# Optimization experiments

Measured on AMD Instinct MI355X. Metric: run time of the kernel, lower is better.

The kernel has to match this reference:

```python
import jax, jax.numpy as jnp
import numpy as np
import math

D_MODEL = 768
HEADS = 12
D_FF = 3072
B, S = 2, 2048


def layer_norm(x, g, b, eps=1e-6):
    mu = jnp.mean(x, axis=-1, keepdims=True)
    var = jnp.mean((x - mu) ** 2, axis=-1, keepdims=True)
    return (x - mu) / jnp.sqrt(var + eps) * g + b


def gelu_tanh(x):
    c = math.sqrt(2.0 / math.pi)
    return 0.5 * x * (1.0 + jnp.tanh(c * (x + 0.044715 * x ** 3)))


def setup_inputs() -> dict:
    key = jax.random.key(0)
    ks = jax.random.split(key, 12)
    s = 0.02
    inp = {
        "iter": 1,
        "query": jax.random.normal(ks[0], (B, S, D_MODEL), jnp.float32),
        "inputs": jax.random.normal(ks[1], (B, S, D_MODEL), jnp.float32),
        "mask": jax.random.randint(ks[2], (B, S), 0, 2).astype(bool),
        "Wq": jax.random.normal(ks[3], (D_MODEL, D_MODEL), jnp.float32) * s,
        "bq": jnp.zeros((D_MODEL,), jnp.float32),
        "Wk": jax.random.normal(ks[4], (D_MODEL, D_MODEL), jnp.float32) * s,
        "bk": jnp.zeros((D_MODEL,), jnp.float32),
        "Wv": jax.random.normal(ks[5], (D_MODEL, D_MODEL), jnp.float32) * s,
        "bv": jnp.zeros((D_MODEL,), jnp.float32),
        "Wo": jax.random.normal(ks[6], (D_MODEL, D_MODEL), jnp.float32) * s,
        "bo": jnp.zeros((D_MODEL,), jnp.float32),
        "ln1_g": jnp.ones((D_MODEL,), jnp.float32),
        "ln1_b": jnp.zeros((D_MODEL,), jnp.float32),
        "W1": jax.random.normal(ks[7], (D_MODEL, D_FF), jnp.float32) * s,
        "b1": jnp.zeros((D_FF,), jnp.float32),
        "W2": jax.random.normal(ks[8], (D_FF, D_MODEL), jnp.float32) * s,
        "b2": jnp.zeros((D_MODEL,), jnp.float32),
        "ln2_g": jnp.ones((D_MODEL,), jnp.float32),
        "ln2_b": jnp.zeros((D_MODEL,), jnp.float32),
    }
    return inp


def reference(iter, query, inputs, mask, Wq, bq, Wk, bk, Wv, bv, Wo, bo,
              ln1_g, ln1_b, W1, b1, W2, b2, ln2_g, ln2_b):
    dh = D_MODEL // HEADS
    # pre-LN (skipped when iter == 0)
    x = layer_norm(inputs, ln1_g, ln1_b) if iter != 0 else inputs
    # QKV projections -> [B, H, S, dh]
    def heads(t):
        return t.reshape(B, S, HEADS, dh).transpose(0, 2, 1, 3)
    q = heads(x @ Wq + bq) / math.sqrt(dh)
    k = heads(x @ Wk + bk)
    v = heads(x @ Wv + bv)
    scores = jnp.einsum("bhqd,bhkd->bhqk", q, k)
    scores = jnp.where(mask[:, None, None, :], -1e18, scores)
    attn = jax.nn.softmax(scores, axis=-1)
    ctx = jnp.einsum("bhqk,bhkd->bhqd", attn, v)
    ctx = ctx.transpose(0, 2, 1, 3).reshape(B, S, D_MODEL)
    attn_out = ctx @ Wo + bo
    out = attn_out + inputs  # dropout=0 -> identity
    # FFN with residual pre-LN and tanh-GELU
    h = layer_norm(out, ln2_g, ln2_b)
    inter = gelu_tanh(h @ W1 + b1)
    return inter @ W2 + b2 + out
```

## Files before the change

### kernel.cpp

```cpp
#include <hip/hip_runtime.h>
#include <hip/hip_bf16.h>
#include <stdint.h>

#define D_MODEL 768
#define HEADS   12
#define DHEAD   64
#define D_FF    3072
#define BB      2
#define SS      2048
#define MTOT    (BB*SS)

typedef uint16_t u16;
typedef uint32_t u32;
typedef __attribute__((ext_vector_type(8))) short short8;
typedef __attribute__((ext_vector_type(4))) short short4v;
typedef __attribute__((ext_vector_type(4))) float f32x4;
typedef __attribute__((ext_vector_type(16))) float f32x16;
typedef __attribute__((ext_vector_type(2))) unsigned uint2v;

__device__ __forceinline__ u16 f2bf(float f) {
    union { float f; u32 u; } v; v.f = f;
    u32 r = v.u + 0x7fffu + ((v.u >> 16) & 1u);
    return (u16)(r >> 16);
}

__device__ __forceinline__ float bf2f(u16 u) {
    union { u32 u; float f; } v; v.u = ((u32)u) << 16;
    return v.f;
}

__device__ __forceinline__ u32 cvtpk(float a, float b) {
    u32 r;
    asm("v_cvt_pk_bf16_f32 %0, %1, %2" : "=v"(r) : "v"(a), "v"(b));
    return r;
}

__device__ __forceinline__ void plswap(u32& a, u32& b, int hi) {
#if __has_builtin(__builtin_amdgcn_permlane32_swap)
    uint2v r = __builtin_amdgcn_permlane32_swap(a, b, false, false);
    a = r[0]; b = r[1];
#else
    u32 ax = (u32)__shfl_xor((int)a, 32), bx = (u32)__shfl_xor((int)b, 32);
    u32 na = hi ? bx : a, nb = hi ? b : ax;
    a = na; b = nb;
#endif
}

__device__ __forceinline__ void gload16(const void* g, void* l) {
    __builtin_amdgcn_global_load_lds(
        (const __attribute__((address_space(1))) u32*)g,
        (__attribute__((address_space(3))) u32*)l, 16, 0, 0);
}

#define MFMA16(a, b, c) __builtin_amdgcn_mfma_f32_16x16x32_bf16((a), (b), (c), 0, 0, 0)
#define MFMA32(a, b, c) __builtin_amdgcn_mfma_f32_32x32x16_bf16((a), (b), (c), 0, 0, 0)

__device__ __forceinline__ float gelu_tanh_f(float x) {
    float x3 = x * x * x;
    return 0.5f * x * (1.0f + tanhf(0.7978845608028654f * (x + 0.044715f * x3)));
}

__global__ __launch_bounds__(256)
void transpose_cast(const float* __restrict__ W, u16* __restrict__ Wt, int R, int C) {
    __shared__ float tile[32][33];
    int bx = blockIdx.x, by = blockIdx.y;
    int x = threadIdx.x & 31, y0 = threadIdx.x >> 5;
#pragma unroll
    for (int i = 0; i < 4; ++i) {
        int y = y0 + i * 8;
        tile[y][x] = W[(size_t)(by * 32 + y) * C + bx * 32 + x];
    }
    __syncthreads();
#pragma unroll
    for (int i = 0; i < 4; ++i) {
        int y = y0 + i * 8;
        Wt[(size_t)(bx * 32 + y) * R + by * 32 + x] = f2bf(tile[x][y]);
    }
}

__global__ void maskprep(const int* __restrict__ m, float* __restrict__ mf, int n) {
    int i = blockIdx.x * 256 + threadIdx.x;
    if (i < n) mf[i] = m[i] ? -1e30f : 0.0f;
}

__global__ __launch_bounds__(256)
void ln_bf16(const float* __restrict__ in, const float* __restrict__ g,
             const float* __restrict__ bta, u16* __restrict__ out,
             const int* __restrict__ iterp, int checkIter) {
    int row = blockIdx.x, tid = threadIdx.x;
    const float* x = in + (size_t)row * D_MODEL;
    float v0 = x[tid], v1 = x[tid + 256], v2 = x[tid + 512];
    float s = v0 + v1 + v2;
    float s2 = v0 * v0 + v1 * v1 + v2 * v2;
#pragma unroll
    for (int o = 1; o < 64; o <<= 1) { s += __shfl_xor(s, o); s2 += __shfl_xor(s2, o); }
    __shared__ float sh[8];
    int w = tid >> 6;
    if ((tid & 63) == 0) { sh[w] = s; sh[4 + w] = s2; }
    __syncthreads();
    s = sh[0] + sh[1] + sh[2] + sh[3];
    s2 = sh[4] + sh[5] + sh[6] + sh[7];
    float mu = s * (1.0f / 768.0f);
    float var = s2 * (1.0f / 768.0f) - mu * mu;
    float rstd = rsqrtf(var + 1e-6f);
    bool skip = checkIter && (iterp[0] == 0);
    u16* o0 = out + (size_t)row * D_MODEL;
    if (skip) {
        o0[tid] = f2bf(v0); o0[tid + 256] = f2bf(v1); o0[tid + 512] = f2bf(v2);
    } else {
        o0[tid]       = f2bf((v0 - mu) * rstd * g[tid]       + bta[tid]);
        o0[tid + 256] = f2bf((v1 - mu) * rstd * g[tid + 256] + bta[tid + 256]);
        o0[tid + 512] = f2bf((v2 - mu) * rstd * g[tid + 512] + bta[tid + 512]);
    }
}

template <int MODE>
__global__ __launch_bounds__(256, 3)
void gemm_bt(const u16* __restrict__ A, const u16* __restrict__ Bt,
             int K, int N,
             const float* __restrict__ bias0, const float* __restrict__ bias1,
             const float* __restrict__ bias2,
             const float* __restrict__ res,
             float* __restrict__ outF, u16* __restrict__ oq,
             u16* __restrict__ ok, u16* __restrict__ ov) {
    __shared__ __align__(16) u16 aT[3][128 * 32];
    __shared__ __align__(16) u16 bT[3][128 * 32];
    const int tid = threadIdx.x;
    const int lane = tid & 63;
    const int w = tid >> 6;
    const int wr = w >> 1, wc = w & 1;
    const int lm = lane & 15, lq = lane >> 4;
    const int bm = blockIdx.y, bn = blockIdx.x;
    const int kzlen = K / gridDim.z;
    const int kbeg = blockIdx.z * kzlen;
    const int nsteps = kzlen >> 5;

    const u16* Abase = A  + (size_t)(bm * 128) * K + kbeg;
    const u16* Bbase = Bt + (size_t)(bn * 128) * K + kbeg;

    auto stage = [&](int buf, int t) {
        int k0 = t * 32;
#pragma unroll
        for (int j = 0; j < 2; ++j) {
            int d = j * 256 + tid;
            int row = d >> 2, p = d & 3;
            int src = (p ^ (row & 3)) * 8;
            gload16(Abase + (size_t)row * K + k0 + src, aT[buf] + (j * 256 + w * 64) * 8);
            gload16(Bbase + (size_t)row * K + k0 + src, bT[buf] + (j * 256 + w * 64) * 8);
        }
    };

    f32x4 acc[4][4] = {};
    stage(0, 0);
    if (nsteps > 1) stage(1, 1);

#pragma unroll 1
    for (int t = 0; t < nsteps; ++t) {
        if (t + 1 < nsteps) asm volatile("s_waitcnt vmcnt(4)" ::: "memory");
        else                asm volatile("s_waitcnt vmcnt(0)" ::: "memory");
        __syncthreads();
        const u16* Ab = aT[t % 3];
        const u16* Bb = bT[t % 3];
        short8 av[4], bv[4];
#pragma unroll
        for (int m = 0; m < 4; ++m) {
            int row = wr * 64 + m * 16 + lm;
            av[m] = *(const short8*)(Ab + row * 32 + ((lq ^ (row & 3)) * 8));
        }
#pragma unroll
        for (int n = 0; n < 4; ++n) {
            int row = wc * 64 + n * 16 + lm;
            bv[n] = *(const short8*)(Bb + row * 32 + ((lq ^ (row & 3)) * 8));
        }
#pragma unroll
        for (int m = 0; m < 4; ++m)
#pragma unroll
            for (int n = 0; n < 4; ++n)
                acc[m][n] = MFMA16(av[m], bv[n], acc[m][n]);
        if (t + 2 < nsteps) stage((t + 2) % 3, t + 2);
    }

#pragma unroll
    for (int m = 0; m < 4; ++m) {
#pragma unroll
        for (int n = 0; n < 4; ++n) {
            int col = bn * 128 + wc * 64 + n * 16 + lm;
#pragma unroll
            for (int r = 0; r < 4; ++r) {
                int row = bm * 128 + wr * 64 + m * 16 + lq * 4 + r;
                float v = acc[m][n][r];
                if (MODE == 0) {
                    int proj = col / D_MODEL;
                    int d = col - proj * D_MODEL;
                    int hh = d >> 6, dhi = d & 63;
                    int bb = row >> 11, sIdx = row & 2047;
                    if (proj == 0) {
                        v = (v + bias0[d]) * 0.18033688011112042f;
                        oq[((size_t)(bb * HEADS + hh) * SS + sIdx) * DHEAD + dhi] = f2bf(v);
                    } else if (proj == 1) {
                        v = v + bias1[d];
                        ok[((size_t)(bb * HEADS + hh) * SS + sIdx) * DHEAD + dhi] = f2bf(v);
                    } else {
                        v = v + bias2[d];
                        ov[((size_t)(bb * HEADS + hh) * DHEAD + dhi) * SS + sIdx] = f2bf(v);
                    }
                } else if (MODE == 1) {
                    if (gridDim.z > 1) {
                        outF[((size_t)blockIdx.z * MTOT + row) * N + col] = v;
                    } else {
                        size_t idx = (size_t)row * N + col;
                        outF[idx] = v + bias0[col] + res[idx];
                    }
                } else {
                    float t2 = v + bias0[col];
                    oq[(size_t)row * N + col] = f2bf(gelu_tanh_f(t2));
                }
            }
        }
    }
}

__global__ __launch_bounds__(256)
void reduce_ks2(const float* __restrict__ pf, const float* __restrict__ bias,
                const float* __restrict__ res, float* __restrict__ out, int N) {
    size_t i = ((size_t)blockIdx.x * 256 + threadIdx.x) * 4;
    f32x4 s0 = *(const f32x4*)(pf + i);
    f32x4 s1 = *(const f32x4*)(pf + (size_t)MTOT * N + i);
    int col = (int)(i % (size_t)N);
    f32x4 b = *(const f32x4*)(bias + col);
    f32x4 r = *(const f32x4*)(res + i);
    f32x4 o;
#pragma unroll
    for (int e = 0; e < 4; ++e) o[e] = s0[e] + s1[e] + b[e] + r[e];
    *(f32x4*)(out + i) = o;
}

__global__ __launch_bounds__(256, 3)
void attn_fwd3(const u16* __restrict__ q, const u16* __restrict__ k,
               const u16* __restrict__ vtg, const float* __restrict__ mkf,
               u16* __restrict__ po, float* __restrict__ pml) {
    __shared__ __align__(16) u16 kls[2][64 * 64];
    __shared__ __align__(16) u16 vls[2][64 * 64];
    __shared__ __align__(16) float mlds[1024];

    const int tid = threadIdx.x, lane = tid & 63, w = tid >> 6;
    const int lm = lane & 31, hi = lane >> 5;
    const int head = blockIdx.y;
    const int bb = head / HEADS;
    const int qblk = blockIdx.x >> 1, chunk = blockIdx.x & 1;
    const int q0 = qblk * 128;
    const int k0 = chunk * 1024;

    const u16* qbase = q + (size_t)head * SS * DHEAD;
    const u16* kbase = k + (size_t)head * SS * DHEAD;
    const u16* vbase = vtg + (size_t)head * DHEAD * SS;
    const float* mrow = mkf + bb * SS;

    short8 qf[4];
    const int qrow = q0 + w * 32 + lm;
#pragma unroll
    for (int c = 0; c < 4; ++c)
        qf[c] = *(const short8*)(qbase + (size_t)qrow * DHEAD + c * 16 + hi * 8);

    gload16(mrow + k0 + tid * 4, mlds + w * 256);

    auto stage = [&](int buf, int t) {
#pragma unroll
        for (int j = 0; j < 2; ++j) {
            int c = j * 256 + tid;
            int row = c >> 3, jj = c & 7;
            gload16(kbase + (size_t)(k0 + t * 64 + row) * DHEAD + ((jj ^ (row & 7)) * 8),
                    kls[buf] + (j * 256 + w * 64) * 8);
            gload16(vbase + (size_t)row * SS + k0 + t * 64 + ((jj ^ (row & 7)) * 8),
                    vls[buf] + (j * 256 + w * 64) * 8);
        }
    };
    stage(0, 0);
    asm volatile("s_waitcnt vmcnt(0)" ::: "memory");
    __syncthreads();

    f32x16 o0 = {}, o1 = {};
    float m = -1e30f, l = 0.0f;
    int cur = 0;

#pragma unroll 1
    for (int t = 0; t < 16; ++t) {
        if (t < 15) stage(cur ^ 1, t + 1);
        const u16* kb = kls[cur];
        const u16* vb = vls[cur];
#pragma unroll
        for (int s = 0; s < 2; ++s) {
            short8 av[4];
#pragma unroll
            for (int c = 0; c < 4; ++c)
                av[c] = *(const short8*)(kb + (s * 32 + lm) * 64 + (((c * 2 + hi) ^ (lm & 7)) * 8));
            short8 vf[4];
#pragma unroll
            for (int kc = 0; kc < 2; ++kc)
#pragma unroll
                for (int df = 0; df < 2; ++df)
                    vf[kc * 2 + df] = *(const short8*)(vb + (df * 32 + lm) * 64 +
                                                       (((s * 4 + kc * 2 + hi) ^ (lm & 7)) * 8));

            f32x16 st = {};
#pragma unroll
            for (int c = 0; c < 4; ++c) st = MFMA32(av[c], qf[c], st);

            float sv[16];
#pragma unroll
            for (int g = 0; g < 4; ++g) {
                f32x4 mk = *(const f32x4*)(mlds + t * 64 + s * 32 + g * 8 + hi * 4);
#pragma unroll
                for (int e = 0; e < 4; ++e) sv[g * 4 + e] = st[g * 4 + e] + mk[e];
            }
            float x0 = fmaxf(sv[0], sv[1]),  x1 = fmaxf(sv[2], sv[3]);
            float x2 = fmaxf(sv[4], sv[5]),  x3 = fmaxf(sv[6], sv[7]);
            float x4 = fmaxf(sv[8], sv[9]),  x5 = fmaxf(sv[10], sv[11]);
            float x6 = fmaxf(sv[12], sv[13]), x7 = fmaxf(sv[14], sv[15]);
            float y0 = fmaxf(x0, x1), y1 = fmaxf(x2, x3);
            float y2 = fmaxf(x4, x5), y3 = fmaxf(x6, x7);
            float pmax = fmaxf(fmaxf(y0, y1), fmaxf(y2, y3));
            pmax = fmaxf(pmax, __shfl_xor(pmax, 32));
            if (__any(pmax > m + 8.0f)) {
                float mn = fmaxf(m, pmax);
                float al = exp2f(m - mn);
                m = mn; l *= al;
#pragma unroll
                for (int r = 0; r < 16; ++r) { o0[r] *= al; o1[r] *= al; }
            }
            float p[16];
#pragma unroll
            for (int r = 0; r < 16; ++r) p[r] = exp2f(sv[r] - m);
            float s0a = (p[0] + p[1]) + (p[2] + p[3]);
            float s1a = (p[4] + p[5]) + (p[6] + p[7]);
            float s2a = (p[8] + p[9]) + (p[10] + p[11]);
            float s3a = (p[12] + p[13]) + (p[14] + p[15]);
            float ls = (s0a + s1a) + (s2a + s3a);
            l += ls + __shfl_xor(ls, 32);

            u32 W[8];
#pragma unroll
            for (int t8 = 0; t8 < 8; ++t8) W[t8] = cvtpk(p[2 * t8], p[2 * t8 + 1]);
            union { u32 wd[4]; short8 s8; } pf0, pf1;
            u32 a0 = W[0], b0 = W[2]; plswap(a0, b0, hi);
            u32 a1 = W[1], b1 = W[3]; plswap(a1, b1, hi);
            u32 a2 = W[4], b2 = W[6]; plswap(a2, b2, hi);
            u32 a3 = W[5], b3 = W[7]; plswap(a3, b3, hi);
            pf0.wd[0] = a0; pf0.wd[1] = a1; pf0.wd[2] = b0; pf0.wd[3] = b1;
            pf1.wd[0] = a2; pf1.wd[1] = a3; pf1.wd[2] = b2; pf1.wd[3] = b3;

            o0 = MFMA32(vf[0], pf0.s8, o0);
            o1 = MFMA32(vf[1], pf0.s8, o1);
            o0 = MFMA32(vf[2], pf1.s8, o0);
            o1 = MFMA32(vf[3], pf1.s8, o1);
        }
        asm volatile("s_waitcnt vmcnt(0)" ::: "memory");
        __syncthreads();
        cur ^= 1;
    }

    const int pc = (head * 16 + qblk) * 2 + chunk;
    u16* orow = po + ((size_t)pc * 128 + (w * 32 + lm)) * 64;
#pragma unroll
    for (int g = 0; g < 4; ++g) {
        short4v pk0, pk1;
#pragma unroll
        for (int e = 0; e < 4; ++e) {
            pk0[e] = (short)f2bf(o0[g * 4 + e]);
            pk1[e] = (short)f2bf(o1[g * 4 + e]);
        }
        *(short4v*)(orow + g * 8 + hi * 4) = pk0;
        *(short4v*)(orow + 32 + g * 8 + hi * 4) = pk1;
    }
    if (hi == 0) {
        float* mlp = pml + ((size_t)pc * 128 + (w * 32 + lm)) * 2;
        mlp[0] = m; mlp[1] = l;
    }
}

__global__ __launch_bounds__(256)
void attn_merge(const u16* __restrict__ po, const float* __restrict__ pml,
                u16* __restrict__ ctx) {
    const int head = blockIdx.y;
    const int bb = head / HEADS, hh = head % HEADS;
    const int rl = threadIdx.x >> 4, dg = threadIdx.x & 15;
    const int s = blockIdx.x * 16 + rl;
    const int qb = s >> 7, qr = s & 127;
    const int pc = (head * 16 + qb) * 2;

    const float* ml1 = pml + ((size_t)pc * 128 + qr) * 2;
    const float* ml2 = ml1 + 128 * 2;
    float m1 = ml1[0], l1 = ml1[1], m2 = ml2[0], l2 = ml2[1];
    float ms = fmaxf(m1, m2);
    float w1 = exp2f(m1 - ms), w2 = exp2f(m2 - ms);
    float inv = 1.0f / (w1 * l1 + w2 * l2);

    const u16* o1p = po + (((size_t)pc * 128 + qr) * 64) + dg * 4;
    const u16* o2p = o1p + 128 * 64;
    short4v a = *(const short4v*)o1p, b = *(const short4v*)o2p;
    short4v r;
#pragma unroll
    for (int e = 0; e < 4; ++e) {
        float v = (bf2f((u16)a[e]) * w1 + bf2f((u16)b[e]) * w2) * inv;
        r[e] = (short)f2bf(v);
    }
    *(short4v*)(ctx + ((size_t)(bb * SS + s)) * D_MODEL + hh * DHEAD + dg * 4) = r;
}

extern "C" void kernel_launch(void* const* d_in, const int* in_sizes, int n_in,
                              void* d_out, int out_size, void* d_ws, size_t ws_size,
                              hipStream_t stream) {
    const int*   iterp  = (const int*)  d_in[0];
    const float* inputs = (const float*)d_in[2];
    const int*   mask   = (const int*)  d_in[3];
    const float* Wq = (const float*)d_in[4];
    const float* bq = (const float*)d_in[5];
    const float* Wk = (const float*)d_in[6];
    const float* bk = (const float*)d_in[7];
    const float* Wv = (const float*)d_in[8];
    const float* bv = (const float*)d_in[9];
    const float* Wo = (const float*)d_in[10];
    const float* bo = (const float*)d_in[11];
    const float* ln1g = (const float*)d_in[12];
    const float* ln1b = (const float*)d_in[13];
    const float* W1 = (const float*)d_in[14];
    const float* b1 = (const float*)d_in[15];
    const float* W2 = (const float*)d_in[16];
    const float* b2 = (const float*)d_in[17];
    const float* ln2g = (const float*)d_in[18];
    const float* ln2b = (const float*)d_in[19];
    float* outp = (float*)d_out;

    char* ws = (char*)d_ws;
    size_t off = 0;
    auto alloc = [&](size_t bytes) -> void* {
        void* p = ws + off;
        off += (bytes + 255) & ~(size_t)255;
        return p;
    };
    u16*   wqkv_t = (u16*)  alloc((size_t)2304 * 768 * 2);
    u16*   wo_t   = (u16*)  alloc((size_t)768 * 768 * 2);
    u16*   w1_t   = (u16*)  alloc((size_t)3072 * 768 * 2);
    u16*   w2_t   = (u16*)  alloc((size_t)768 * 3072 * 2);
    float* mkf    = (float*)alloc((size_t)MTOT * 4);
    u16*   xh     = (u16*)  alloc((size_t)MTOT * 768 * 2);
    u16*   qb     = (u16*)  alloc((size_t)MTOT * 768 * 2);
    u16*   kbuf   = (u16*)  alloc((size_t)MTOT * 768 * 2);
    u16*   vtb    = (u16*)  alloc((size_t)MTOT * 768 * 2);
    u16*   ctxb   = (u16*)  alloc((size_t)MTOT * 768 * 2);
    float* outm   = (float*)alloc((size_t)MTOT * 768 * 4);
    u16*   inter  = qb;

    u16*   po  = (u16*)outm;
    float* pml = (float*)xh;

    float* pfbuf = (float*)alloc((size_t)2 * MTOT * 768 * 4);
    const bool split_ok = (off <= ws_size);

    dim3 blk(256);
    transpose_cast<<<dim3(24, 24), blk, 0, stream>>>(Wq, wqkv_t,                 768, 768);
    transpose_cast<<<dim3(24, 24), blk, 0, stream>>>(Wk, wqkv_t + 768 * 768,     768, 768);
    transpose_cast<<<dim3(24, 24), blk, 0, stream>>>(Wv, wqkv_t + 2 * 768 * 768, 768, 768);
    transpose_cast<<<dim3(24, 24), blk, 0, stream>>>(Wo, wo_t, 768, 768);
    transpose_cast<<<dim3(96, 24), blk, 0, stream>>>(W1, w1_t, 768, 3072);
    transpose_cast<<<dim3(24, 96), blk, 0, stream>>>(W2, w2_t, 3072, 768);
    maskprep<<<dim3(16), blk, 0, stream>>>(mask, mkf, MTOT);

    ln_bf16<<<dim3(MTOT), blk, 0, stream>>>(inputs, ln1g, ln1b, xh, iterp, 1);

    gemm_bt<0><<<dim3(2304 / 128, MTOT / 128), blk, 0, stream>>>(
        xh, wqkv_t, 768, 2304, bq, bk, bv, nullptr, nullptr, qb, kbuf, vtb);

    attn_fwd3<<<dim3(32, BB * HEADS), dim3(256), 0, stream>>>(
        qb, kbuf, vtb, mkf, po, pml);
    attn_merge<<<dim3(SS / 16, BB * HEADS), dim3(256), 0, stream>>>(po, pml, ctxb);

    if (split_ok) {
        gemm_bt<1><<<dim3(768 / 128, MTOT / 128, 2), blk, 0, stream>>>(
            ctxb, wo_t, 768, 768, nullptr, nullptr, nullptr, nullptr,
            pfbuf, nullptr, nullptr, nullptr);
        reduce_ks2<<<dim3(MTOT * 768 / 1024), blk, 0, stream>>>(pfbuf, bo, inputs, outm, 768);
    } else {
        gemm_bt<1><<<dim3(768 / 128, MTOT / 128), blk, 0, stream>>>(
            ctxb, wo_t, 768, 768, bo, nullptr, nullptr, inputs, outm, nullptr, nullptr, nullptr);
    }

    ln_bf16<<<dim3(MTOT), blk, 0, stream>>>(outm, ln2g, ln2b, xh, iterp, 0);

    gemm_bt<2><<<dim3(3072 / 128, MTOT / 128), blk, 0, stream>>>(
        xh, w1_t, 768, 3072, b1, nullptr, nullptr, nullptr, nullptr, inter, nullptr, nullptr);

    if (split_ok) {
        gemm_bt<1><<<dim3(768 / 128, MTOT / 128, 2), blk, 0, stream>>>(
            inter, w2_t, 3072, 768, nullptr, nullptr, nullptr, nullptr,
            pfbuf, nullptr, nullptr, nullptr);
        reduce_ks2<<<dim3(MTOT * 768 / 1024), blk, 0, stream>>>(pfbuf, b2, outm, outp, 768);
    } else {
        gemm_bt<1><<<dim3(768 / 128, MTOT / 128), blk, 0, stream>>>(
            inter, w2_t, 3072, 768, b2, nullptr, nullptr, outm, outp, nullptr, nullptr, nullptr);
    }
}
```

Before: 249.6 us.

## Fold key mask into V and MFMA row sums; fuse split-K reduce with LayerNorm

The key mask is no longer added to attention scores as -1e30. V rows for masked keys are zeroed in the QKV GEMM epilogue, and the softmax denominator is computed by an MFMA of the bf16 0/1 mask against P. This removes per-element mask adds and the shuffle-based row-sum reduction from the attention inner loop. Separately, the split-K reduce of the output projection is fused with the second LayerNorm, so one kernel launch and a full re-read of the residual buffer go away. Masked keys still enter the running max, which can change numerics (for example a fully masked row now divides by zero), and bf16 P adds rounding to the denominator.

```diff
diff --git a/kernel.cpp b/kernel.cpp
--- a/kernel.cpp
+++ b/kernel.cpp
@@ -78,9 +78,14 @@
     }
 }
 
-__global__ void maskprep(const int* __restrict__ m, float* __restrict__ mf, int n) {
+__global__ void maskprep(const int* __restrict__ m, float* __restrict__ vz,
+                         u16* __restrict__ m01, int n) {
     int i = blockIdx.x * 256 + threadIdx.x;
-    if (i < n) mf[i] = m[i] ? -1e30f : 0.0f;
+    if (i < n) {
+        float v = m[i] ? 0.0f : 1.0f;
+        vz[i] = v;
+        m01[i] = f2bf(v);
+    }
 }
 
 __global__ __launch_bounds__(256)
@@ -112,6 +117,37 @@
         o0[tid + 256] = f2bf((v1 - mu) * rstd * g[tid + 256] + bta[tid + 256]);
         o0[tid + 512] = f2bf((v2 - mu) * rstd * g[tid + 512] + bta[tid + 512]);
     }
+}
+
+__global__ __launch_bounds__(256)
+void ln_fuse(const float* __restrict__ pf, const float* __restrict__ bias,
+             const float* __restrict__ res, const float* __restrict__ g,
+             const float* __restrict__ bta, float* __restrict__ outm,
+             u16* __restrict__ out) {
+    int row = blockIdx.x, tid = threadIdx.x;
+    size_t i0 = (size_t)row * D_MODEL + tid;
+    const float* pf1 = pf + (size_t)MTOT * D_MODEL;
+    float v0 = pf[i0]       + pf1[i0]       + bias[tid]       + res[i0];
+    float v1 = pf[i0 + 256] + pf1[i0 + 256] + bias[tid + 256] + res[i0 + 256];
+    float v2 = pf[i0 + 512] + pf1[i0 + 512] + bias[tid + 512] + res[i0 + 512];
+    outm[i0] = v0; outm[i0 + 256] = v1; outm[i0 + 512] = v2;
+    float s = v0 + v1 + v2;
+    float s2 = v0 * v0 + v1 * v1 + v2 * v2;
+#pragma unroll
+    for (int o = 1; o < 64; o <<= 1) { s += __shfl_xor(s, o); s2 += __shfl_xor(s2, o); }
+    __shared__ float sh[8];
+    int w = tid >> 6;
+    if ((tid & 63) == 0) { sh[w] = s; sh[4 + w] = s2; }
+    __syncthreads();
+    s = sh[0] + sh[1] + sh[2] + sh[3];
+    s2 = sh[4] + sh[5] + sh[6] + sh[7];
+    float mu = s * (1.0f / 768.0f);
+    float var = s2 * (1.0f / 768.0f) - mu * mu;
+    float rstd = rsqrtf(var + 1e-6f);
+    u16* o0 = out + (size_t)row * D_MODEL;
+    o0[tid]       = f2bf((v0 - mu) * rstd * g[tid]       + bta[tid]);
+    o0[tid + 256] = f2bf((v1 - mu) * rstd * g[tid + 256] + bta[tid + 256]);
+    o0[tid + 512] = f2bf((v2 - mu) * rstd * g[tid + 512] + bta[tid + 512]);
 }
 
 template <int MODE>
@@ -201,7 +237,7 @@
                         v = v + bias1[d];
                         ok[((size_t)(bb * HEADS + hh) * SS + sIdx) * DHEAD + dhi] = f2bf(v);
                     } else {
-                        v = v + bias2[d];
+                        v = (v + bias2[d]) * res[row];
                         ov[((size_t)(bb * HEADS + hh) * DHEAD + dhi) * SS + sIdx] = f2bf(v);
                     }
                 } else if (MODE == 1) {
@@ -237,11 +273,11 @@
 
 __global__ __launch_bounds__(256, 3)
 void attn_fwd3(const u16* __restrict__ q, const u16* __restrict__ k,
-               const u16* __restrict__ vtg, const float* __restrict__ mkf,
+               const u16* __restrict__ vtg, const u16* __restrict__ m01g,
                u16* __restrict__ po, float* __restrict__ pml) {
     __shared__ __align__(16) u16 kls[2][64 * 64];
     __shared__ __align__(16) u16 vls[2][64 * 64];
-    __shared__ __align__(16) float mlds[1024];
+    __shared__ __align__(16) u16 m01l[1024];
 
     const int tid = threadIdx.x, lane = tid & 63, w = tid >> 6;
     const int lm = lane & 31, hi = lane >> 5;
@@ -254,7 +290,7 @@
     const u16* qbase = q + (size_t)head * SS * DHEAD;
     const u16* kbase = k + (size_t)head * SS * DHEAD;
     const u16* vbase = vtg + (size_t)head * DHEAD * SS;
-    const float* mrow = mkf + bb * SS;
+    const u16* m01row = m01g + bb * SS;
 
     short8 qf[4];
     const int qrow = q0 + w * 32 + lm;
@@ -262,7 +298,7 @@
     for (int c = 0; c < 4; ++c)
         qf[c] = *(const short8*)(qbase + (size_t)qrow * DHEAD + c * 16 + hi * 8);
 
-    gload16(mrow + k0 + tid * 4, mlds + w * 256);
+    if (w < 2) gload16(m01row + k0 + (size_t)tid * 8, m01l + (size_t)w * 64 * 8);
 
     auto stage = [&](int buf, int t) {
 #pragma unroll
@@ -279,8 +315,8 @@
     asm volatile("s_waitcnt vmcnt(0)" ::: "memory");
     __syncthreads();
 
-    f32x16 o0 = {}, o1 = {};
-    float m = -1e30f, l = 0.0f;
+    f32x16 o0 = {}, o1 = {}, accl = {};
+    float m = -1e30f;
     int cur = 0;
 
 #pragma unroll 1
@@ -301,54 +337,47 @@
                 for (int df = 0; df < 2; ++df)
                     vf[kc * 2 + df] = *(const short8*)(vb + (df * 32 + lm) * 64 +
                                                        (((s * 4 + kc * 2 + hi) ^ (lm & 7)) * 8));
+            short8 mf0 = *(const short8*)(m01l + t * 64 + s * 32 + hi * 8);
+            short8 mf1 = *(const short8*)(m01l + t * 64 + s * 32 + 16 + hi * 8);
 
             f32x16 st = {};
 #pragma unroll
             for (int c = 0; c < 4; ++c) st = MFMA32(av[c], qf[c], st);
 
-            float sv[16];
-#pragma unroll
-            for (int g = 0; g < 4; ++g) {
-                f32x4 mk = *(const f32x4*)(mlds + t * 64 + s * 32 + g * 8 + hi * 4);
-#pragma unroll
-                for (int e = 0; e < 4; ++e) sv[g * 4 + e] = st[g * 4 + e] + mk[e];
-            }
-            float x0 = fmaxf(sv[0], sv[1]),  x1 = fmaxf(sv[2], sv[3]);
-            float x2 = fmaxf(sv[4], sv[5]),  x3 = fmaxf(sv[6], sv[7]);
-            float x4 = fmaxf(sv[8], sv[9]),  x5 = fmaxf(sv[10], sv[11]);
-            float x6 = fmaxf(sv[12], sv[13]), x7 = fmaxf(sv[14], sv[15]);
-            float y0 = fmaxf(x0, x1), y1 = fmaxf(x2, x3);
-            float y2 = fmaxf(x4, x5), y3 = fmaxf(x6, x7);
-            float pmax = fmaxf(fmaxf(y0, y1), fmaxf(y2, y3));
+            float a0 = fmaxf(fmaxf(st[0],  st[1]),  st[2]);
+            float a1 = fmaxf(fmaxf(st[3],  st[4]),  st[5]);
+            float a2 = fmaxf(fmaxf(st[6],  st[7]),  st[8]);
+            float a3 = fmaxf(fmaxf(st[9],  st[10]), st[11]);
+            float a4 = fmaxf(fmaxf(st[12], st[13]), st[14]);
+            float b0 = fmaxf(fmaxf(a0, a1), a2);
+            float b1 = fmaxf(fmaxf(a3, a4), st[15]);
+            float pmax = fmaxf(b0, b1);
             pmax = fmaxf(pmax, __shfl_xor(pmax, 32));
             if (__any(pmax > m + 8.0f)) {
                 float mn = fmaxf(m, pmax);
                 float al = exp2f(m - mn);
-                m = mn; l *= al;
+                m = mn;
 #pragma unroll
                 for (int r = 0; r < 16; ++r) { o0[r] *= al; o1[r] *= al; }
+                accl[0] *= al;
             }
             float p[16];
 #pragma unroll
-            for (int r = 0; r < 16; ++r) p[r] = exp2f(sv[r] - m);
-            float s0a = (p[0] + p[1]) + (p[2] + p[3]);
-            float s1a = (p[4] + p[5]) + (p[6] + p[7]);
-            float s2a = (p[8] + p[9]) + (p[10] + p[11]);
-            float s3a = (p[12] + p[13]) + (p[14] + p[15]);
-            float ls = (s0a + s1a) + (s2a + s3a);
-            l += ls + __shfl_xor(ls, 32);
+            for (int r = 0; r < 16; ++r) p[r] = exp2f(st[r] - m);
 
             u32 W[8];
 #pragma unroll
             for (int t8 = 0; t8 < 8; ++t8) W[t8] = cvtpk(p[2 * t8], p[2 * t8 + 1]);
             union { u32 wd[4]; short8 s8; } pf0, pf1;
-            u32 a0 = W[0], b0 = W[2]; plswap(a0, b0, hi);
-            u32 a1 = W[1], b1 = W[3]; plswap(a1, b1, hi);
-            u32 a2 = W[4], b2 = W[6]; plswap(a2, b2, hi);
-            u32 a3 = W[5], b3 = W[7]; plswap(a3, b3, hi);
-            pf0.wd[0] = a0; pf0.wd[1] = a1; pf0.wd[2] = b0; pf0.wd[3] = b1;
-            pf1.wd[0] = a2; pf1.wd[1] = a3; pf1.wd[2] = b2; pf1.wd[3] = b3;
-
+            u32 a0w = W[0], b0w = W[2]; plswap(a0w, b0w, hi);
+            u32 a1w = W[1], b1w = W[3]; plswap(a1w, b1w, hi);
+            u32 a2w = W[4], b2w = W[6]; plswap(a2w, b2w, hi);
+            u32 a3w = W[5], b3w = W[7]; plswap(a3w, b3w, hi);
+            pf0.wd[0] = a0w; pf0.wd[1] = a1w; pf0.wd[2] = b0w; pf0.wd[3] = b1w;
+            pf1.wd[0] = a2w; pf1.wd[1] = a3w; pf1.wd[2] = b2w; pf1.wd[3] = b3w;
+
+            accl = MFMA32(mf0, pf0.s8, accl);
+            accl = MFMA32(mf1, pf1.s8, accl);
             o0 = MFMA32(vf[0], pf0.s8, o0);
             o1 = MFMA32(vf[1], pf0.s8, o1);
             o0 = MFMA32(vf[2], pf1.s8, o0);
@@ -374,7 +403,7 @@
     }
     if (hi == 0) {
         float* mlp = pml + ((size_t)pc * 128 + (w * 32 + lm)) * 2;
-        mlp[0] = m; mlp[1] = l;
+        mlp[0] = m; mlp[1] = accl[0];
     }
 }
 
@@ -442,7 +471,8 @@
     u16*   wo_t   = (u16*)  alloc((size_t)768 * 768 * 2);
     u16*   w1_t   = (u16*)  alloc((size_t)3072 * 768 * 2);
     u16*   w2_t   = (u16*)  alloc((size_t)768 * 3072 * 2);
-    float* mkf    = (float*)alloc((size_t)MTOT * 4);
+    float* vzf    = (float*)alloc((size_t)MTOT * 4);
+    u16*   m01    = (u16*)  alloc((size_t)MTOT * 2);
     u16*   xh     = (u16*)  alloc((size_t)MTOT * 768 * 2);
     u16*   qb     = (u16*)  alloc((size_t)MTOT * 768 * 2);
     u16*   kbuf   = (u16*)  alloc((size_t)MTOT * 768 * 2);
@@ -464,28 +494,27 @@
     transpose_cast<<<dim3(24, 24), blk, 0, stream>>>(Wo, wo_t, 768, 768);
     transpose_cast<<<dim3(96, 24), blk, 0, stream>>>(W1, w1_t, 768, 3072);
     transpose_cast<<<dim3(24, 96), blk, 0, stream>>>(W2, w2_t, 3072, 768);
-    maskprep<<<dim3(16), blk, 0, stream>>>(mask, mkf, MTOT);
+    maskprep<<<dim3(16), blk, 0, stream>>>(mask, vzf, m01, MTOT);
 
     ln_bf16<<<dim3(MTOT), blk, 0, stream>>>(inputs, ln1g, ln1b, xh, iterp, 1);
 
     gemm_bt<0><<<dim3(2304 / 128, MTOT / 128), blk, 0, stream>>>(
-        xh, wqkv_t, 768, 2304, bq, bk, bv, nullptr, nullptr, qb, kbuf, vtb);
+        xh, wqkv_t, 768, 2304, bq, bk, bv, vzf, nullptr, qb, kbuf, vtb);
 
     attn_fwd3<<<dim3(32, BB * HEADS), dim3(256), 0, stream>>>(
-        qb, kbuf, vtb, mkf, po, pml);
+        qb, kbuf, vtb, m01, po, pml);
     attn_merge<<<dim3(SS / 16, BB * HEADS), dim3(256), 0, stream>>>(po, pml, ctxb);
 
     if (split_ok) {
         gemm_bt<1><<<dim3(768 / 128, MTOT / 128, 2), blk, 0, stream>>>(
             ctxb, wo_t, 768, 768, nullptr, nullptr, nullptr, nullptr,
             pfbuf, nullptr, nullptr, nullptr);
-        reduce_ks2<<<dim3(MTOT * 768 / 1024), blk, 0, stream>>>(pfbuf, bo, inputs, outm, 768);
+        ln_fuse<<<dim3(MTOT), blk, 0, stream>>>(pfbuf, bo, inputs, ln2g, ln2b, outm, xh);
     } else {
         gemm_bt<1><<<dim3(768 / 128, MTOT / 128), blk, 0, stream>>>(
             ctxb, wo_t, 768, 768, bo, nullptr, nullptr, inputs, outm, nullptr, nullptr, nullptr);
-    }
-
-    ln_bf16<<<dim3(MTOT), blk, 0, stream>>>(outm, ln2g, ln2b, xh, iterp, 0);
+        ln_bf16<<<dim3(MTOT), blk, 0, stream>>>(outm, ln2g, ln2b, xh, iterp, 0);
+    }
 
     gemm_bt<2><<<dim3(3072 / 128, MTOT / 128), blk, 0, stream>>>(
         xh, w1_t, 768, 3072, b1, nullptr, nullptr, nullptr, nullptr, inter, nullptr, nullptr);
```

After: 239.8 us. 1.04x faster.
